# Optimization experiments

Measured on AMD Instinct MI355X. Metric: run time of the kernel, lower is better.

Reference implementation:

```python
import jax, jax.numpy as jnp
import numpy as np

BN_EPS = 1e-5
MIN_DIST = 1e-10


def _conv_bn_relu(x, w, b, gamma, beta):
    # pointwise Conv1d (kernel=1) == per-point linear, then BatchNorm1d (training-mode
    # batch stats, biased variance, as torch does for normalization), then ReLU.
    y = jnp.einsum('oc,bcn->bon', w, x) + b[None, :, None]
    mu = y.mean(axis=(0, 2))
    var = y.var(axis=(0, 2))
    yn = (y - mu[None, :, None]) * jax.lax.rsqrt(var + BN_EPS)[None, :, None]
    return jax.nn.relu(yn * gamma[None, :, None] + beta[None, :, None])


def setup_inputs() -> dict:
    key = jax.random.key(0)
    ks = jax.random.split(key, 12)
    B, N1, N2, C1, C2 = 8, 8192, 2048, 128, 256
    in_ch = C1 + C2  # 384
    mlp = [256, 128]
    inp = {
        'xyz1': jax.random.normal(ks[0], (B, N1, 3), jnp.float32),
        'xyz2': jax.random.normal(ks[1], (B, N2, 3), jnp.float32),
        'points1': jax.random.normal(ks[2], (B, C1, N1), jnp.float32),
        'points2': jax.random.normal(ks[3], (B, C2, N2), jnp.float32),
    }
    last = in_ch
    for i, out_ch in enumerate(mlp):
        scale = 1.0 / np.sqrt(last)
        inp[f'w{i}'] = jax.random.uniform(ks[4 + 2 * i], (out_ch, last), jnp.float32, -scale, scale)
        inp[f'b{i}'] = jax.random.uniform(ks[5 + 2 * i], (out_ch,), jnp.float32, -scale, scale)
        inp[f'gamma{i}'] = jnp.ones((out_ch,), jnp.float32)
        inp[f'beta{i}'] = jnp.zeros((out_ch,), jnp.float32)
        last = out_ch
    return inp


def reference(xyz1, xyz2, points1, points2,
              w0, b0, gamma0, beta0, w1, b1, gamma1, beta1):
    # Euclidean distance matrix [B, N1, N2] (torch.cdist, p=2)
    sq = (jnp.sum(xyz1 * xyz1, -1)[:, :, None]
          + jnp.sum(xyz2 * xyz2, -1)[:, None, :]
          - 2.0 * jnp.einsum('bnd,bmd->bnm', xyz1, xyz2))
    dists = jnp.sqrt(jnp.maximum(sq, 0.0))
    # 3 smallest distances + indices (ascending, matching torch.topk largest=False)
    neg_d, knn_idx = jax.lax.top_k(-dists, 3)  # [B, N1, 3]
    knn_d = jnp.maximum(-neg_d, MIN_DIST)
    weights = 1.0 / knn_d
    weights = weights / jnp.sum(weights, axis=2, keepdims=True)  # [B, N1, 3]
    # gather neighbor features: points2 [B, C2, N2] -> [B, C2, N1, 3]
    knn_feats = jnp.take_along_axis(points2[:, :, None, :],
                                    knn_idx[:, None, :, :], axis=3)
    interpolated = jnp.sum(knn_feats * weights[:, None, :, :], axis=3)  # [B, C2, N1]
    new_points = jnp.concatenate([points1, interpolated], axis=1)  # [B, C1+C2, N1]
    new_points = _conv_bn_relu(new_points, w0, b0, gamma0, beta0)
    new_points = _conv_bn_relu(new_points, w1, b1, gamma1, beta1)
    return new_points
```

## Files before the change

kernel.cpp:

```cpp
#include <hip/hip_runtime.h>
#include <cstdint>

using u16 = unsigned short;
typedef short bf16x8 __attribute__((ext_vector_type(8)));
typedef float f32x4 __attribute__((ext_vector_type(4)));

__device__ __forceinline__ float bf2f(u16 h) {
    union { unsigned u; float f; } x;
    x.u = ((unsigned)h) << 16;
    return x.f;
}
__device__ __forceinline__ u16 f2bf(float f) {
    union { float f; unsigned u; } x;
    x.f = f;
    unsigned r = x.u + 0x7fffu + ((x.u >> 16) & 1u);
    return (u16)(r >> 16);
}

__device__ __forceinline__ void gl_lds16(const u16* g, u16* l) {
    __builtin_amdgcn_global_load_lds((const __attribute__((address_space(1))) void*)g,
                                     (__attribute__((address_space(3))) void*)l, 16, 0, 0);
}

#define N1 8192
#define N2 2048
#define C2 256

__device__ __forceinline__ void tr_tile(const float* __restrict__ src,
                                        u16* __restrict__ dst,
                                        int C, int N, int ds, int b, int n0, int c0,
                                        int tid, float (*tile)[33]) {
    int tx = tid & 31, ty = tid >> 5;
    const float* s = src + (long)b * C * N;
#pragma unroll
    for (int i = 0; i < 4; i++) {
        int c = ty + i * 8;
        tile[c][tx] = s[(long)(c0 + c) * N + n0 + tx];
    }
    __syncthreads();
    u16* d = dst + (long)b * N * ds;
#pragma unroll
    for (int i = 0; i < 4; i++) {
        int n = ty + i * 8;
        d[(long)(n0 + n) * ds + c0 + tx] = f2bf(tile[tx][n]);
    }
}

__global__ __launch_bounds__(256) void preproc(const float* __restrict__ w0,
                                               const float* __restrict__ w1,
                                               const float* __restrict__ points2,
                                               u16* __restrict__ w0b,
                                               u16* __restrict__ w1b,
                                               u16* __restrict__ P2T,
                                               float* __restrict__ stats) {
    __shared__ float tile[32][33];
    int bid = blockIdx.x, tid = threadIdx.x;
    if (bid < 4096) {
        int nb = bid & 63, cb = (bid >> 6) & 7, b = bid >> 9;
        tr_tile(points2, P2T, 256, 2048, 256, b, nb * 32, cb * 32, tid, tile);
    } else if (bid < 4480) {
        int i = (bid - 4096) * 256 + tid;
        w0b[i] = f2bf(w0[i]);
    } else if (bid < 4608) {
        int i = (bid - 4480) * 256 + tid;
        w1b[i] = f2bf(w1[i]);
    } else {
        for (int i = tid; i < 768; i += 256) stats[i] = 0.0f;
    }
}

__global__ __launch_bounds__(512) void knn_interp(const float* __restrict__ xyz1,
                                                  const float* __restrict__ xyz2,
                                                  const float* __restrict__ points1,
                                                  const u16* __restrict__ P2T,
                                                  u16* __restrict__ X) {
    __shared__ float4 pts[N2 / 2 + 16];
    __shared__ float m_d[8][64][3];
    __shared__ int   m_i[8][64][3];
    __shared__ int   s_idx[64][3];
    __shared__ float s_w[64][3];
    int b = blockIdx.y;
    int n0 = blockIdx.x * 64;
    int tid = threadIdx.x;
    int ql = tid & 63;
    int part = tid >> 6;

    int cp = tid >> 3;
    int g = tid & 7;
    const float* p1r0 = points1 + ((long)b * 128 + 2 * cp) * N1 + n0 + g * 8;
    const float* p1r1 = p1r0 + N1;
    float4 c0a = *(const float4*)(p1r0);
    float4 c0b = *(const float4*)(p1r0 + 4);
    float4 c1a = *(const float4*)(p1r1);
    float4 c1b = *(const float4*)(p1r1 + 4);
    asm volatile("" ::: "memory");

    int n = n0 + ql;
    float px = xyz1[((long)b * N1 + n) * 3 + 0];
    float py = xyz1[((long)b * N1 + n) * 3 + 1];
    float pz = xyz1[((long)b * N1 + n) * 3 + 2];
    float psq = __fadd_rn(__fadd_rn(__fmul_rn(px, px), __fmul_rn(py, py)), __fmul_rn(pz, pz));

    float b0 = 1e30f, b1 = 1e30f, b2 = 1e30f;
    int i0 = 0, i1 = 0, i2 = 0;

    for (int half = 0; half < 2; half++) {
        for (int j = tid; j < N2 / 2; j += 512) {
            int jg = half * (N2 / 2) + j;
            float x = xyz2[((long)b * N2 + jg) * 3 + 0];
            float y = xyz2[((long)b * N2 + jg) * 3 + 1];
            float z = xyz2[((long)b * N2 + jg) * 3 + 2];
            float nsq = __fadd_rn(__fadd_rn(__fmul_rn(x, x), __fmul_rn(y, y)), __fmul_rn(z, z));
            pts[j] = make_float4(x, y, z, nsq);
        }
        __syncthreads();

        int jbeg = half * (N2 / 2) + part * (N2 / 16);
        const float4* lp = &pts[part * (N2 / 16)];
#pragma unroll 8
        for (int jj = 0; jj < N2 / 16; jj++) {
            int j = jbeg + jj;
            float4 p = lp[jj];
            float dot = __fadd_rn(__fadd_rn(__fmul_rn(px, p.x), __fmul_rn(py, p.y)),
                                  __fmul_rn(pz, p.z));
            float sq = __fsub_rn(__fadd_rn(psq, p.w), __fmul_rn(2.0f, dot));
            if (sq < b2) {
                if (sq < b1) {
                    b2 = b1; i2 = i1;
                    if (sq < b0) { b1 = b0; i1 = i0; b0 = sq; i0 = j; }
                    else         { b1 = sq; i1 = j; }
                } else { b2 = sq; i2 = j; }
            }
        }
        __syncthreads();
    }

    m_d[part][ql][0] = b0; m_d[part][ql][1] = b1; m_d[part][ql][2] = b2;
    m_i[part][ql][0] = i0; m_i[part][ql][1] = i1; m_i[part][ql][2] = i2;
    __syncthreads();

    {
        unsigned* t32 = (unsigned*)pts;
        float r0[8] = {c0a.x, c0a.y, c0a.z, c0a.w, c0b.x, c0b.y, c0b.z, c0b.w};
        float r1[8] = {c1a.x, c1a.y, c1a.z, c1a.w, c1b.x, c1b.y, c1b.z, c1b.w};
#pragma unroll
        for (int k = 0; k < 8; k++) {
            unsigned v = (unsigned)f2bf(r0[k]) | ((unsigned)f2bf(r1[k]) << 16);
            t32[(g * 8 + k) * 65 + cp] = v;
        }
    }

    if (tid < 64) {
        float c0 = 1e30f, c1 = 1e30f, c2 = 1e30f;
        int a0 = 0x7fffffff, a1 = 0x7fffffff, a2 = 0x7fffffff;
#pragma unroll
        for (int pp = 0; pp < 8; pp++) {
#pragma unroll
            for (int k = 0; k < 3; k++) {
                float d = m_d[pp][tid][k];
                int ix = m_i[pp][tid][k];
                if (d < c2 || (d == c2 && ix < a2)) {
                    if (d < c1 || (d == c1 && ix < a1)) {
                        c2 = c1; a2 = a1;
                        if (d < c0 || (d == c0 && ix < a0)) { c1 = c0; a1 = a0; c0 = d; a0 = ix; }
                        else                                { c1 = d; a1 = ix; }
                    } else { c2 = d; a2 = ix; }
                }
            }
        }
        float e0 = sqrtf(fmaxf(c0, 0.0f));
        float e1 = sqrtf(fmaxf(c1, 0.0f));
        float e2 = sqrtf(fmaxf(c2, 0.0f));
        float kd0 = fmaxf(e0, 1e-10f), kd1 = fmaxf(e1, 1e-10f), kd2 = fmaxf(e2, 1e-10f);
        float w0 = __fdiv_rn(1.0f, kd0), w1 = __fdiv_rn(1.0f, kd1), w2 = __fdiv_rn(1.0f, kd2);
        float wsum = __fadd_rn(__fadd_rn(w0, w1), w2);
        s_idx[tid][0] = a0; s_idx[tid][1] = a1; s_idx[tid][2] = a2;
        s_w[tid][0] = __fdiv_rn(w0, wsum);
        s_w[tid][1] = __fdiv_rn(w1, wsum);
        s_w[tid][2] = __fdiv_rn(w2, wsum);
    }
    __syncthreads();

    {
        const unsigned* t32 = (const unsigned*)pts;
        int p = tid >> 3, ch = tid & 7;
        unsigned v[8];
#pragma unroll
        for (int j = 0; j < 8; j++) v[j] = t32[p * 65 + ch * 8 + j];
        uint4* xo = (uint4*)(X + (long)(b * N1 + n0 + p) * 384);
        xo[ch * 2]     = make_uint4(v[0], v[1], v[2], v[3]);
        xo[ch * 2 + 1] = make_uint4(v[4], v[5], v[6], v[7]);
    }

    int l = tid & 63;
    const u16* base = P2T + (long)b * N2 * C2;
#pragma unroll 2
    for (int p = part; p < 64; p += 8) {
        int j0 = s_idx[p][0], j1 = s_idx[p][1], j2 = s_idx[p][2];
        float f0 = s_w[p][0], f1 = s_w[p][1], f2 = s_w[p][2];
        ushort4 r0 = *(const ushort4*)&base[(long)j0 * C2 + l * 4];
        ushort4 r1 = *(const ushort4*)&base[(long)j1 * C2 + l * 4];
        ushort4 r2 = *(const ushort4*)&base[(long)j2 * C2 + l * 4];
        ushort4 o;
        o.x = f2bf(__fadd_rn(__fadd_rn(__fmul_rn(bf2f(r0.x), f0), __fmul_rn(bf2f(r1.x), f1)),
                             __fmul_rn(bf2f(r2.x), f2)));
        o.y = f2bf(__fadd_rn(__fadd_rn(__fmul_rn(bf2f(r0.y), f0), __fmul_rn(bf2f(r1.y), f1)),
                             __fmul_rn(bf2f(r2.y), f2)));
        o.z = f2bf(__fadd_rn(__fadd_rn(__fmul_rn(bf2f(r0.z), f0), __fmul_rn(bf2f(r1.z), f1)),
                             __fmul_rn(bf2f(r2.z), f2)));
        o.w = f2bf(__fadd_rn(__fadd_rn(__fmul_rn(bf2f(r0.w), f0), __fmul_rn(bf2f(r1.w), f1)),
                             __fmul_rn(bf2f(r2.w), f2)));
        *(ushort4*)&X[(long)(b * N1 + n0 + p) * 384 + 128 + l * 4] = o;
    }
}

template <int KDIM, bool BN_IN, bool ASYNC, bool SWZ>
__global__ __launch_bounds__(256) void gemm_bn(const u16* __restrict__ A,
                                               const u16* __restrict__ Bw,
                                               const float* __restrict__ bias,
                                               const float* __restrict__ g_in_sum,
                                               const float* __restrict__ g_in_ssq,
                                               const float* __restrict__ gamma_in,
                                               const float* __restrict__ beta_in,
                                               u16* __restrict__ Yout, int Ntot,
                                               float* __restrict__ g_out_sum,
                                               float* __restrict__ g_out_ssq) {
    constexpr int LDSZ = ASYNC ? 2 * 128 * 32 : 128 * 40;
    constexpr int SUB = 128 * 32;
    __shared__ __align__(16) u16 Al[LDSZ];
    __shared__ __align__(16) u16 Bl[LDSZ];
    __shared__ float s_stats[256];
    __shared__ float s_scale[BN_IN ? KDIM : 2];
    __shared__ float s_shift[BN_IN ? KDIM : 2];

    int tid = threadIdx.x;
    long s0;
    int o0;
    if constexpr (SWZ) {
        int bid = blockIdx.x;
        int xcd = bid & 7;
        int i = bid >> 3;
        int u = xcd * 64 + (i >> 1);
        s0 = (long)u * 128;
        o0 = (i & 1) * 128;
    } else {
        s0 = (long)blockIdx.y * 128;
        o0 = blockIdx.x * 128;
    }

    s_stats[tid] = 0.0f;
    if constexpr (BN_IN) {
        for (int k = tid; k < KDIM; k += 256) {
            float mu = g_in_sum[k] * (1.0f / 65536.0f);
            float var = g_in_ssq[k] * (1.0f / 65536.0f) - mu * mu;
            float rs = rsqrtf(var + 1e-5f);
            float sc = gamma_in[k] * rs;
            s_scale[k] = sc;
            s_shift[k] = beta_in[k] - mu * sc;
        }
    }
    int wid = tid >> 6, lane = tid & 63;
    int wm = wid >> 1, wn = wid & 1;
    int q = lane >> 4, l16 = lane & 15;

    f32x4 acc[4][4];
#pragma unroll
    for (int mi = 0; mi < 4; mi++)
#pragma unroll
        for (int ni = 0; ni < 4; ni++) acc[mi][ni] = (f32x4){0.f, 0.f, 0.f, 0.f};

    int rbase0 = wid * 32;
    int rsub = lane >> 2;
    int colsw = (((lane & 3) ^ (rsub & 3)) << 3);
    const u16* gA0 = A + (s0 + rbase0 + rsub) * KDIM + colsw;
    const u16* gA1 = gA0 + (long)16 * KDIM;
    const u16* gB0 = Bw + (long)(o0 + rbase0 + rsub) * KDIM + colsw;
    const u16* gB1 = gB0 + (long)16 * KDIM;
    u16* lA0 = &Al[rbase0 * 32];
    u16* lA1 = &Al[(rbase0 + 16) * 32];
    u16* lB0 = &Bl[rbase0 * 32];
    u16* lB1 = &Bl[(rbase0 + 16) * 32];
    int qA = ASYNC ? (q ^ (l16 & 3)) : q;

    __syncthreads();

    if constexpr (ASYNC) {
        for (int kt = 0; kt < KDIM; kt += 64) {
#pragma unroll
            for (int sub = 0; sub < 2; sub++) {
                int ko = kt + sub * 32;
                gl_lds16(gA0 + ko, lA0 + sub * SUB);
                gl_lds16(gA1 + ko, lA1 + sub * SUB);
                gl_lds16(gB0 + ko, lB0 + sub * SUB);
                gl_lds16(gB1 + ko, lB1 + sub * SUB);
            }
            __syncthreads();
#pragma unroll
            for (int sub = 0; sub < 2; sub++) {
                bf16x8 af[4], bfr[4];
#pragma unroll
                for (int mi = 0; mi < 4; mi++)
                    af[mi] = *(const bf16x8*)&Al[sub * SUB + (wm * 64 + mi * 16 + l16) * 32 + qA * 8];
#pragma unroll
                for (int ni = 0; ni < 4; ni++)
                    bfr[ni] = *(const bf16x8*)&Bl[sub * SUB + (wn * 64 + ni * 16 + l16) * 32 + qA * 8];
#pragma unroll
                for (int mi = 0; mi < 4; mi++)
#pragma unroll
                    for (int ni = 0; ni < 4; ni++)
                        acc[mi][ni] = __builtin_amdgcn_mfma_f32_16x16x32_bf16(af[mi], bfr[ni],
                                                                              acc[mi][ni], 0, 0, 0);
            }
            __syncthreads();
        }
    } else {
        for (int kt = 0; kt < KDIM; kt += 32) {
#pragma unroll
            for (int cc = 0; cc < 2; cc++) {
                int ci = tid + cc * 256;
                int row = ci >> 2;
                int kc = (ci & 3) << 3;
                union { uint4 u; u16 h[8]; } va;
                va.u = *(const uint4*)(A + (s0 + row) * KDIM + kt + kc);
                if constexpr (BN_IN) {
#pragma unroll
                    for (int j = 0; j < 8; j++) {
                        float f = bf2f(va.h[j]);
                        f = fmaxf(fmaf(f, s_scale[kt + kc + j], s_shift[kt + kc + j]), 0.0f);
                        va.h[j] = f2bf(f);
                    }
                }
                *(uint4*)&Al[row * 40 + kc] = va.u;
                *(uint4*)&Bl[row * 40 + kc] = *(const uint4*)(Bw + (long)(o0 + row) * KDIM + kt + kc);
            }
            __syncthreads();
            bf16x8 af[4], bfr[4];
#pragma unroll
            for (int mi = 0; mi < 4; mi++)
                af[mi] = *(const bf16x8*)&Al[(wm * 64 + mi * 16 + l16) * 40 + qA * 8];
#pragma unroll
            for (int ni = 0; ni < 4; ni++)
                bfr[ni] = *(const bf16x8*)&Bl[(wn * 64 + ni * 16 + l16) * 40 + qA * 8];
#pragma unroll
            for (int mi = 0; mi < 4; mi++)
#pragma unroll
                for (int ni = 0; ni < 4; ni++)
                    acc[mi][ni] = __builtin_amdgcn_mfma_f32_16x16x32_bf16(af[mi], bfr[ni],
                                                                          acc[mi][ni], 0, 0, 0);
            __syncthreads();
        }
    }

#pragma unroll
    for (int ni = 0; ni < 4; ni++) {
        int coll = wn * 64 + ni * 16 + l16;
        int col = o0 + coll;
        float bz = bias[col];
        float s1 = 0.0f, s2 = 0.0f;
#pragma unroll
        for (int mi = 0; mi < 4; mi++) {
#pragma unroll
            for (int r = 0; r < 4; r++) {
                float v = acc[mi][ni][r] + bz;
                s1 += v;
                s2 += v * v;
                long row = s0 + wm * 64 + mi * 16 + q * 4 + r;
                Yout[row * Ntot + col] = f2bf(v);
            }
        }
        s1 += __shfl_xor(s1, 16, 64);
        s1 += __shfl_xor(s1, 32, 64);
        s2 += __shfl_xor(s2, 16, 64);
        s2 += __shfl_xor(s2, 32, 64);
        if (q == 0) {
            atomicAdd(&s_stats[coll], s1);
            atomicAdd(&s_stats[128 + coll], s2);
        }
    }
    __syncthreads();
    if (tid < 128) {
        atomicAdd(&g_out_sum[o0 + tid], s_stats[tid]);
        atomicAdd(&g_out_ssq[o0 + tid], s_stats[128 + tid]);
    }
}

__global__ __launch_bounds__(256) void finalize_k(const u16* __restrict__ Y1,
                                                  const float* __restrict__ g_sum,
                                                  const float* __restrict__ g_ssq,
                                                  const float* __restrict__ gamma,
                                                  const float* __restrict__ beta,
                                                  float* __restrict__ out) {
    __shared__ float s_scale[128], s_shift[128];
    int tid = threadIdx.x;
    if (tid < 128) {
        float mu = g_sum[tid] * (1.0f / 65536.0f);
        float var = g_ssq[tid] * (1.0f / 65536.0f) - mu * mu;
        float rs = rsqrtf(var + 1e-5f);
        float sc = gamma[tid] * rs;
        s_scale[tid] = sc;
        s_shift[tid] = beta[tid] - mu * sc;
    }
    __syncthreads();
    long s = (long)blockIdx.x * 256 + tid;
    int b = (int)(s >> 13);
    int n = (int)(s & 8191);
    const u16* yrow = Y1 + s * 128;
    float* obase = out + (long)b * 128 * 8192 + n;
#pragma unroll
    for (int oc = 0; oc < 128; oc += 8) {
        union { uint4 u; u16 h[8]; } va;
        va.u = *(const uint4*)&yrow[oc];
#pragma unroll
        for (int k = 0; k < 8; k++) {
            int o = oc + k;
            float v = fmaxf(fmaf(bf2f(va.h[k]), s_scale[o], s_shift[o]), 0.0f);
            obase[(long)o * 8192] = v;
        }
    }
}

extern "C" void kernel_launch(void* const* d_in, const int* in_sizes, int n_in,
                              void* d_out, int out_size, void* d_ws, size_t ws_size,
                              hipStream_t stream) {
    const float* xyz1    = (const float*)d_in[0];
    const float* xyz2    = (const float*)d_in[1];
    const float* points1 = (const float*)d_in[2];
    const float* points2 = (const float*)d_in[3];
    const float* w0 = (const float*)d_in[4];
    const float* b0 = (const float*)d_in[5];
    const float* gamma0 = (const float*)d_in[6];
    const float* beta0 = (const float*)d_in[7];
    const float* w1 = (const float*)d_in[8];
    const float* b1 = (const float*)d_in[9];
    const float* gamma1 = (const float*)d_in[10];
    const float* beta1 = (const float*)d_in[11];
    float* out = (float*)d_out;

    char* ws = (char*)d_ws;
    u16* X       = (u16*)(ws + 0);
    u16* P2T     = (u16*)(ws + 50331648);
    u16* w0b     = (u16*)(ws + 58720256);
    u16* w1b     = (u16*)(ws + 58916864);
    u16* Y0      = (u16*)(ws + 58982400);
    u16* Y1b     = (u16*)(ws + 92536832);
    float* stats = (float*)(ws + 109314048);
    if (ws_size < 109317120) return;
    float* gsum0 = stats;
    float* gss0  = stats + 256;
    float* gsum1 = stats + 512;
    float* gss1  = stats + 640;

    preproc<<<4609, 256, 0, stream>>>(w0, w1, points2, w0b, w1b, P2T, stats);
    knn_interp<<<dim3(128, 8), 512, 0, stream>>>(xyz1, xyz2, points1, P2T, X);
    gemm_bn<384, false, true, true><<<1024, 256, 0, stream>>>(
        X, w0b, b0, nullptr, nullptr, nullptr, nullptr, Y0, 256, gsum0, gss0);
    gemm_bn<256, true, false, false><<<dim3(1, 512), 256, 0, stream>>>(
        Y0, w1b, b1, gsum0, gss0, gamma0, beta0, Y1b, 128, gsum1, gss1);
    finalize_k<<<256, 256, 0, stream>>>(Y1b, gsum1, gss1, gamma1, beta1, out);
}
```

Measured before the change: 243.0 us.

## Fuse final BN+ReLU into second GEMM via grid-wide barrier

The second GEMM no longer writes its bf16 output to memory. Each block joins an atomic-counter grid barrier until every block has added its column statistics, then computes BN scale and shift and writes the normalized, ReLU'd fp32 output directly from registers through an LDS transpose. This removes the finalize kernel, its launch, and a round trip of the intermediate tensor. It relies on all 512 blocks being co-resident (launch bounds raised to 2 blocks per SM), otherwise the spin-wait deadlocks.

```diff
diff --git a/kernel.cpp b/kernel.cpp
--- a/kernel.cpp
+++ b/kernel.cpp
@@ -52,7 +52,8 @@
                                                u16* __restrict__ w0b,
                                                u16* __restrict__ w1b,
                                                u16* __restrict__ P2T,
-                                               float* __restrict__ stats) {
+                                               float* __restrict__ stats,
+                                               unsigned* __restrict__ ctr) {
     __shared__ float tile[32][33];
     int bid = blockIdx.x, tid = threadIdx.x;
     if (bid < 4096) {
@@ -66,6 +67,8 @@
         w1b[i] = f2bf(w1[i]);
     } else {
         for (int i = tid; i < 768; i += 256) stats[i] = 0.0f;
+        if (tid == 0)
+            __hip_atomic_store(ctr, 0u, __ATOMIC_RELAXED, __HIP_MEMORY_SCOPE_AGENT);
     }
 }
 
@@ -214,17 +217,21 @@
     }
 }
 
-template <int KDIM, bool BN_IN, bool ASYNC, bool SWZ>
-__global__ __launch_bounds__(256) void gemm_bn(const u16* __restrict__ A,
-                                               const u16* __restrict__ Bw,
-                                               const float* __restrict__ bias,
-                                               const float* __restrict__ g_in_sum,
-                                               const float* __restrict__ g_in_ssq,
-                                               const float* __restrict__ gamma_in,
-                                               const float* __restrict__ beta_in,
-                                               u16* __restrict__ Yout, int Ntot,
-                                               float* __restrict__ g_out_sum,
-                                               float* __restrict__ g_out_ssq) {
+template <int KDIM, bool BN_IN, bool ASYNC, bool SWZ, bool FUSE>
+__global__ __launch_bounds__(256, 2) void gemm_bn(const u16* __restrict__ A,
+                                                  const u16* __restrict__ Bw,
+                                                  const float* __restrict__ bias,
+                                                  const float* __restrict__ g_in_sum,
+                                                  const float* __restrict__ g_in_ssq,
+                                                  const float* __restrict__ gamma_in,
+                                                  const float* __restrict__ beta_in,
+                                                  u16* __restrict__ Yout, int Ntot,
+                                                  float* __restrict__ g_out_sum,
+                                                  float* __restrict__ g_out_ssq,
+                                                  const float* __restrict__ gamma_out,
+                                                  const float* __restrict__ beta_out,
+                                                  float* __restrict__ out,
+                                                  unsigned* __restrict__ ctr) {
     constexpr int LDSZ = ASYNC ? 2 * 128 * 32 : 128 * 40;
     constexpr int SUB = 128 * 32;
     __shared__ __align__(16) u16 Al[LDSZ];
@@ -351,11 +358,13 @@
         }
     }
 
+    float bzs[4];
 #pragma unroll
     for (int ni = 0; ni < 4; ni++) {
         int coll = wn * 64 + ni * 16 + l16;
         int col = o0 + coll;
         float bz = bias[col];
+        bzs[ni] = bz;
         float s1 = 0.0f, s2 = 0.0f;
 #pragma unroll
         for (int mi = 0; mi < 4; mi++) {
@@ -364,8 +373,10 @@
                 float v = acc[mi][ni][r] + bz;
                 s1 += v;
                 s2 += v * v;
-                long row = s0 + wm * 64 + mi * 16 + q * 4 + r;
-                Yout[row * Ntot + col] = f2bf(v);
+                if constexpr (!FUSE) {
+                    long row = s0 + wm * 64 + mi * 16 + q * 4 + r;
+                    Yout[row * Ntot + col] = f2bf(v);
+                }
             }
         }
         s1 += __shfl_xor(s1, 16, 64);
@@ -382,39 +393,61 @@
         atomicAdd(&g_out_sum[o0 + tid], s_stats[tid]);
         atomicAdd(&g_out_ssq[o0 + tid], s_stats[128 + tid]);
     }
-}
-
-__global__ __launch_bounds__(256) void finalize_k(const u16* __restrict__ Y1,
-                                                  const float* __restrict__ g_sum,
-                                                  const float* __restrict__ g_ssq,
-                                                  const float* __restrict__ gamma,
-                                                  const float* __restrict__ beta,
-                                                  float* __restrict__ out) {
-    __shared__ float s_scale[128], s_shift[128];
-    int tid = threadIdx.x;
-    if (tid < 128) {
-        float mu = g_sum[tid] * (1.0f / 65536.0f);
-        float var = g_ssq[tid] * (1.0f / 65536.0f) - mu * mu;
-        float rs = rsqrtf(var + 1e-5f);
-        float sc = gamma[tid] * rs;
-        s_scale[tid] = sc;
-        s_shift[tid] = beta[tid] - mu * sc;
-    }
-    __syncthreads();
-    long s = (long)blockIdx.x * 256 + tid;
-    int b = (int)(s >> 13);
-    int n = (int)(s & 8191);
-    const u16* yrow = Y1 + s * 128;
-    float* obase = out + (long)b * 128 * 8192 + n;
-#pragma unroll
-    for (int oc = 0; oc < 128; oc += 8) {
-        union { uint4 u; u16 h[8]; } va;
-        va.u = *(const uint4*)&yrow[oc];
-#pragma unroll
-        for (int k = 0; k < 8; k++) {
-            int o = oc + k;
-            float v = fmaxf(fmaf(bf2f(va.h[k]), s_scale[o], s_shift[o]), 0.0f);
-            obase[(long)o * 8192] = v;
+
+    if constexpr (FUSE) {
+        __shared__ float tbuf[32][129];
+        __syncthreads();
+        if (tid == 0) {
+            __threadfence();
+            atomicAdd(ctr, 1u);
+            while (__hip_atomic_load(ctr, __ATOMIC_ACQUIRE, __HIP_MEMORY_SCOPE_AGENT)
+                   < gridDim.y)
+                __builtin_amdgcn_s_sleep(2);
+        }
+        __syncthreads();
+        if (tid < 128) {
+            float su = __hip_atomic_load(&g_out_sum[tid], __ATOMIC_RELAXED,
+                                         __HIP_MEMORY_SCOPE_AGENT);
+            float sq = __hip_atomic_load(&g_out_ssq[tid], __ATOMIC_RELAXED,
+                                         __HIP_MEMORY_SCOPE_AGENT);
+            float mu = su * (1.0f / 65536.0f);
+            float var = sq * (1.0f / 65536.0f) - mu * mu;
+            float rs = rsqrtf(var + 1e-5f);
+            float sc = gamma_out[tid] * rs;
+            s_stats[tid] = sc;
+            s_stats[128 + tid] = beta_out[tid] - mu * sc;
+        }
+        __syncthreads();
+        int b = (int)(s0 >> 13);
+        int nb = (int)(s0 & 8191);
+        for (int c = 0; c < 4; c++) {
+            if (wn == (c >> 1)) {
+#pragma unroll
+                for (int nis = 0; nis < 2; nis++) {
+                    int ni = (c & 1) * 2 + nis;
+                    int coll = wn * 64 + ni * 16 + l16;
+                    float sc = s_stats[coll], sh = s_stats[128 + coll];
+                    float bz = bzs[ni];
+#pragma unroll
+                    for (int mi = 0; mi < 4; mi++)
+#pragma unroll
+                        for (int r = 0; r < 4; r++) {
+                            float v = fmaxf(fmaf(acc[mi][ni][r] + bz, sc, sh), 0.0f);
+                            tbuf[nis * 16 + l16][wm * 64 + mi * 16 + q * 4 + r] = v;
+                        }
+                }
+            }
+            __syncthreads();
+            {
+                int cl = tid >> 3, seg = tid & 7;
+                const float* tr = &tbuf[cl][seg * 16];
+                float* orow = out + ((long)b * 128 + c * 32 + cl) * 8192 + nb + seg * 16;
+#pragma unroll
+                for (int j = 0; j < 4; j++)
+                    *(float4*)(orow + j * 4) =
+                        make_float4(tr[j * 4], tr[j * 4 + 1], tr[j * 4 + 2], tr[j * 4 + 3]);
+            }
+            __syncthreads();
         }
     }
 }
@@ -442,7 +475,7 @@
     u16* w0b     = (u16*)(ws + 58720256);
     u16* w1b     = (u16*)(ws + 58916864);
     u16* Y0      = (u16*)(ws + 58982400);
-    u16* Y1b     = (u16*)(ws + 92536832);
+    unsigned* ctr = (unsigned*)(ws + 92536832);
     float* stats = (float*)(ws + 109314048);
     if (ws_size < 109317120) return;
     float* gsum0 = stats;
@@ -450,11 +483,12 @@
     float* gsum1 = stats + 512;
     float* gss1  = stats + 640;
 
-    preproc<<<4609, 256, 0, stream>>>(w0, w1, points2, w0b, w1b, P2T, stats);
+    preproc<<<4609, 256, 0, stream>>>(w0, w1, points2, w0b, w1b, P2T, stats, ctr);
     knn_interp<<<dim3(128, 8), 512, 0, stream>>>(xyz1, xyz2, points1, P2T, X);
-    gemm_bn<384, false, true, true><<<1024, 256, 0, stream>>>(
-        X, w0b, b0, nullptr, nullptr, nullptr, nullptr, Y0, 256, gsum0, gss0);
-    gemm_bn<256, true, false, false><<<dim3(1, 512), 256, 0, stream>>>(
-        Y0, w1b, b1, gsum0, gss0, gamma0, beta0, Y1b, 128, gsum1, gss1);
-    finalize_k<<<256, 256, 0, stream>>>(Y1b, gsum1, gss1, gamma1, beta1, out);
-}
+    gemm_bn<384, false, true, true, false><<<1024, 256, 0, stream>>>(
+        X, w0b, b0, nullptr, nullptr, nullptr, nullptr, Y0, 256, gsum0, gss0,
+        nullptr, nullptr, nullptr, nullptr);
+    gemm_bn<256, true, false, false, true><<<dim3(1, 512), 256, 0, stream>>>(
+        Y0, w1b, b1, gsum0, gss0, gamma0, beta0, nullptr, 128, gsum1, gss1,
+        gamma1, beta1, out, ctr);
+}
```

Result: slower. 278.3 us (+14.5%).

## Double-buffer async LDS loads in GEMM to overlap prefetch with MFMA

Applied to the files above, without the earlier changes.

Restructures the async GEMM main loop from load-64-then-compute into a two-stage ping-pong pipeline over 32-wide K slices. The next slice's global-to-LDS loads are issued before computing on the current one, with explicit vmcnt waits and raw s_barrier replacing __syncthreads. This aims to hide global load latency behind MFMA work. It depends on the hand-set vmcnt counts and sched_barriers being correct, and it adds a barrier per 32-K step.

```diff
diff --git a/kernel.cpp b/kernel.cpp
--- a/kernel.cpp
+++ b/kernel.cpp
@@ -285,33 +285,42 @@
     __syncthreads();
 
     if constexpr (ASYNC) {
-        for (int kt = 0; kt < KDIM; kt += 64) {
-#pragma unroll
-            for (int sub = 0; sub < 2; sub++) {
-                int ko = kt + sub * 32;
-                gl_lds16(gA0 + ko, lA0 + sub * SUB);
-                gl_lds16(gA1 + ko, lA1 + sub * SUB);
-                gl_lds16(gB0 + ko, lB0 + sub * SUB);
-                gl_lds16(gB1 + ko, lB1 + sub * SUB);
+        constexpr int NT = KDIM / 32;
+        gl_lds16(gA0, lA0);
+        gl_lds16(gA1, lA1);
+        gl_lds16(gB0, lB0);
+        gl_lds16(gB1, lB1);
+#pragma unroll 2
+        for (int t = 0; t < NT; t++) {
+            int cur = t & 1;
+            if (t + 1 < NT) {
+                int ko = (t + 1) * 32;
+                int nx = cur ^ 1;
+                gl_lds16(gA0 + ko, lA0 + nx * SUB);
+                gl_lds16(gA1 + ko, lA1 + nx * SUB);
+                gl_lds16(gB0 + ko, lB0 + nx * SUB);
+                gl_lds16(gB1 + ko, lB1 + nx * SUB);
+                asm volatile("s_waitcnt vmcnt(4)" ::: "memory");
+            } else {
+                asm volatile("s_waitcnt vmcnt(0)" ::: "memory");
             }
-            __syncthreads();
-#pragma unroll
-            for (int sub = 0; sub < 2; sub++) {
-                bf16x8 af[4], bfr[4];
-#pragma unroll
-                for (int mi = 0; mi < 4; mi++)
-                    af[mi] = *(const bf16x8*)&Al[sub * SUB + (wm * 64 + mi * 16 + l16) * 32 + qA * 8];
+            __builtin_amdgcn_s_barrier();
+            __builtin_amdgcn_sched_barrier(0);
+            bf16x8 af[4], bfr[4];
+#pragma unroll
+            for (int mi = 0; mi < 4; mi++)
+                af[mi] = *(const bf16x8*)&Al[cur * SUB + (wm * 64 + mi * 16 + l16) * 32 + qA * 8];
+#pragma unroll
+            for (int ni = 0; ni < 4; ni++)
+                bfr[ni] = *(const bf16x8*)&Bl[cur * SUB + (wn * 64 + ni * 16 + l16) * 32 + qA * 8];
+#pragma unroll
+            for (int mi = 0; mi < 4; mi++)
 #pragma unroll
                 for (int ni = 0; ni < 4; ni++)
-                    bfr[ni] = *(const bf16x8*)&Bl[sub * SUB + (wn * 64 + ni * 16 + l16) * 32 + qA * 8];
-#pragma unroll
-                for (int mi = 0; mi < 4; mi++)
-#pragma unroll
-                    for (int ni = 0; ni < 4; ni++)
-                        acc[mi][ni] = __builtin_amdgcn_mfma_f32_16x16x32_bf16(af[mi], bfr[ni],
-                                                                              acc[mi][ni], 0, 0, 0);
-            }
-            __syncthreads();
+                    acc[mi][ni] = __builtin_amdgcn_mfma_f32_16x16x32_bf16(af[mi], bfr[ni],
+                                                                          acc[mi][ni], 0, 0, 0);
+            __builtin_amdgcn_sched_barrier(0);
+            __builtin_amdgcn_s_barrier();
         }
     } else {
         for (int kt = 0; kt < KDIM; kt += 32) {
```

New measurement: 246.5 us. Within noise of the previous version (+1.4%).
